# Kernel optimization log

Hardware: AMD Instinct MI355X
Metric: run time of the kernel (lower is better)

## Reference

```python
import jax, jax.numpy as jnp
import numpy as np

N = 1024          # number of rois (single image)
C = 1024          # in_channels
G = 16            # num_groups
PE = 64           # position_embedding_channels
WAVE_LENGTH = 1000.0


def _position_embedding(bboxes, pe_channels, wave_length):
    # bboxes: [N, 4] xyxy. Pairwise geometric features vs all (nongt == all) boxes.
    x1, y1, x2, y2 = jnp.split(bboxes, 4, axis=1)          # each [N,1]
    cx = (x1 + x2) * 0.5
    cy = (y1 + y2) * 0.5
    w = x2 - x1 + 1.0
    h = y2 - y1 + 1.0
    dX = jnp.log(jnp.clip(jnp.abs((cx - cx.T) / w), 1e-3))  # [N,N]
    dY = jnp.log(jnp.clip(jnp.abs((cy - cy.T) / h), 1e-3))
    dW = jnp.log(w / w.T)
    dH = jnp.log(h / h.T)
    pm = jnp.stack([dX, dY, dW, dH], axis=-1)               # [N,N,4]
    feat_range = jnp.arange(pe_channels // 8, dtype=pm.dtype)
    dim_mat = jnp.power(jnp.asarray(wave_length, pm.dtype),
                        (8.0 / pe_channels) * feat_range)    # [pe//8]
    div = (100.0 * pm)[..., None] / dim_mat                  # [N,N,4,pe//8]
    emb = jnp.concatenate([jnp.sin(div), jnp.cos(div)], axis=3)  # [N,N,4,pe//4]
    return emb.reshape(emb.shape[0], emb.shape[1], -1)       # [N,N,pe]


def setup_inputs() -> dict:
    key = jax.random.key(0)
    ks = jax.random.split(key, 10)
    feats = jax.random.normal(ks[0], (N, C), dtype=jnp.float32)
    # realistic boxes: x1,y1 in [0,800), w,h in [1,200)
    x1 = jax.random.uniform(ks[1], (N, 1), minval=0.0, maxval=800.0)
    y1 = jax.random.uniform(ks[2], (N, 1), minval=0.0, maxval=800.0)
    bw = jax.random.uniform(ks[3], (N, 1), minval=1.0, maxval=200.0)
    bh = jax.random.uniform(ks[4], (N, 1), minval=1.0, maxval=200.0)
    rois = jnp.concatenate([jnp.zeros((N, 1)), x1, y1, x1 + bw, y1 + bh], axis=1).astype(jnp.float32)
    Wq = 0.01 * jax.random.normal(ks[5], (C, C), dtype=jnp.float32)
    bq = jnp.zeros((C,), jnp.float32)
    Wk = 0.01 * jax.random.normal(ks[6], (C, C), dtype=jnp.float32)
    bk = jnp.zeros((C,), jnp.float32)
    Wg = 0.01 * jax.random.normal(ks[7], (G, PE), dtype=jnp.float32)   # 1x1 conv PE->G
    bg = jnp.zeros((G,), jnp.float32)
    # grouped 1x1 conv: in=G*C, out=C, groups=G -> weight [C, C]
    limit = np.sqrt(6.0 / (C + C))
    Wv = jax.random.uniform(ks[8], (C, C), minval=-limit, maxval=limit, dtype=jnp.float32)
    bv = jnp.zeros((C,), jnp.float32)
    return {"feats": feats, "rois": rois, "Wq": Wq, "bq": bq, "Wk": Wk, "bk": bk,
            "Wg": Wg, "bg": bg, "Wv": Wv, "bv": bv}


def reference(feats, rois, Wq, bq, Wk, bk, Wg, bg, Wv, bv):
    n, c = feats.shape
    g = Wg.shape[0]
    gc = c // g
    # position embedding computed under no_grad in torch
    emb = jax.lax.stop_gradient(_position_embedding(rois[:, 1:5], Wg.shape[1], WAVE_LENGTH))  # [N,N,PE]
    # 1x1 conv w_g + relu -> geometric attention weight [N, G, M]
    aff_weight = jax.nn.relu(jnp.einsum('nmp,gp->ngm', emb, Wg) + bg[None, :, None])
    q = (feats @ Wq.T + bq).reshape(n, g, gc)   # [N,G,gc]
    k = (feats @ Wk.T + bk).reshape(n, g, gc)   # [M,G,gc] (nongt == all)
    scale = 1.0 / jnp.sqrt(jnp.asarray(gc, jnp.float32))
    aff = jnp.einsum('ngc,mgc->ngm', q, k) * scale            # [N,G,M]
    weighted = jnp.log(jnp.clip(aff_weight, 1e-6)) + aff
    sm = jax.nn.softmax(weighted, axis=2)                      # [N,G,M]
    out = jnp.einsum('ngm,mc->ngc', sm, feats)                 # [N,G,C]
    # grouped 1x1 conv w_v: group g maps its C-dim aggregate to gc channels
    Wv_g = Wv.reshape(g, gc, c)
    rel = jnp.einsum('ngc,gdc->ngd', out, Wv_g).reshape(n, c) + bv
    return rel
```

## Files before the change

### kernel.cpp

```cpp
#include <hip/hip_runtime.h>
#include <math.h>

#define N_ROIS 1024
#define C_DIM  1024

typedef __attribute__((ext_vector_type(8))) short short8;
typedef __attribute__((ext_vector_type(4))) float f32x4;

__device__ __forceinline__ unsigned short f2bf(float x) {
    union { float f; unsigned u; } v; v.f = x;
    unsigned r = v.u + 0x7fffu + ((v.u >> 16) & 1u);
    return (unsigned short)(r >> 16);
}
__device__ __forceinline__ float bf2f(unsigned short u) {
    return __uint_as_float((unsigned)u << 16);
}
__device__ __forceinline__ unsigned cvtpk(float lo, float hi) {
    unsigned r;
    asm("v_cvt_pk_bf16_f32 %0, %1, %2" : "=v"(r) : "v"(lo), "v"(hi));
    return r;
}
__device__ __forceinline__ float sin_rev(float rev) {
    return __builtin_amdgcn_sinf(__builtin_amdgcn_fractf(rev));
}

__global__ __launch_bounds__(256) void cvt_kernel(
    const float* __restrict__ s0, const float* __restrict__ s1,
    const float* __restrict__ s2, const float* __restrict__ s3,
    unsigned short* __restrict__ d0, unsigned short* __restrict__ d1,
    unsigned short* __restrict__ d2, unsigned short* __restrict__ d3)
{
    const float* s; unsigned short* d;
    switch (blockIdx.y) {
        case 0:  s = s0; d = d0; break;
        case 1:  s = s1; d = d1; break;
        case 2:  s = s2; d = d2; break;
        default: s = s3; d = d3; break;
    }
    const int i = (blockIdx.x * 256 + threadIdx.x) * 8;
    float4 a = *(const float4*)&s[i];
    float4 b = *(const float4*)&s[i + 4];
    uint4 o;
    o.x = cvtpk(a.x, a.y); o.y = cvtpk(a.z, a.w);
    o.z = cvtpk(b.x, b.y); o.w = cvtpk(b.z, b.w);
    *(uint4*)&d[i] = o;
}

struct Triples {
    const unsigned short* A[3];
    const unsigned short* B[3];
    unsigned short*       C[3];
    const float*          bias[3];
};

__global__ __launch_bounds__(256) void prep_kernel(
    Triples tr, const float* __restrict__ rois, const float* __restrict__ Wg,
    const float* __restrict__ bg, unsigned short* __restrict__ logw)
{
    __shared__ __align__(16) char smem[24576];
    const int bx = blockIdx.x;
    const int t  = threadIdx.x;
    const int grp = bx / 11, rem = bx % 11;

    if (rem < 3) {
        const int gid = grp * 3 + rem;
        const int z   = gid >> 7;
        const int r3  = gid & 127;
        const int m0 = (r3 >> 3) * 64, n0 = (r3 & 7) * 128;
        const unsigned short* A = tr.A[z];
        const unsigned short* B = tr.B[z];

        const int lane = t & 63, w = t >> 6;
        const int lx = lane & 15, qw = lane >> 4;

#define PGLD(srcp, dstoff) __builtin_amdgcn_global_load_lds( \
        (const __attribute__((address_space(1))) void*)(srcp), \
        (__attribute__((address_space(3))) void*)(smem + (dstoff)), 16, 0, 0)

        const int rsub = lane >> 2;
        const int sg   = ((lane & 3) ^ (rsub & 3)) * 8;
#define STAGE(bb, kk) do { \
        PGLD(A + (size_t)(m0 + w * 16 + rsub) * 1024 + (kk) + sg, \
             (bb) * 4096 + w * 1024 + lane * 16); \
        PGLD(B + (size_t)(n0 + w * 32 + rsub) * 1024 + (kk) + sg, \
             8192 + (bb) * 8192 + (w * 2) * 1024 + lane * 16); \
        PGLD(B + (size_t)(n0 + w * 32 + 16 + rsub) * 1024 + (kk) + sg, \
             8192 + (bb) * 8192 + (w * 2 + 1) * 1024 + lane * 16); \
    } while (0)

        f32x4 acc[2][4];
        const f32x4 z4 = {0.f, 0.f, 0.f, 0.f};
#pragma unroll
        for (int i = 0; i < 2; ++i)
#pragma unroll
            for (int j = 0; j < 4; ++j) acc[i][j] = z4;

        const int wm = (w & 1) * 32, wn = (w >> 1) * 64;
        const int rdsw = (qw ^ (lx & 3)) << 4;

        STAGE(0, 0);
        __syncthreads();

        for (int k0 = 0; k0 < 1024; k0 += 32) {
            const int cur = (k0 >> 5) & 1;
            if (k0 + 32 < 1024) STAGE(cur ^ 1, k0 + 32);
            const char* Ac = smem + cur * 4096;
            const char* Bc = smem + 8192 + cur * 8192;
            short8 af[2], bfr[4];
#pragma unroll
            for (int mi = 0; mi < 2; ++mi)
                af[mi] = *(const short8*)(Ac + (wm + mi * 16 + lx) * 64 + rdsw);
#pragma unroll
            for (int ni = 0; ni < 4; ++ni)
                bfr[ni] = *(const short8*)(Bc + (wn + ni * 16 + lx) * 64 + rdsw);
#pragma unroll
            for (int mi = 0; mi < 2; ++mi)
#pragma unroll
                for (int ni = 0; ni < 4; ++ni)
                    acc[mi][ni] = __builtin_amdgcn_mfma_f32_16x16x32_bf16(
                        af[mi], bfr[ni], acc[mi][ni], 0, 0, 0);
            __syncthreads();
        }
#undef STAGE
#undef PGLD

        const float* bias = tr.bias[z];
        unsigned short* C = tr.C[z];
        const float sc = (z == 0) ? 0.125f : 1.0f;
        const int r0 = qw * 4, cc = lx;
#pragma unroll
        for (int mi = 0; mi < 2; ++mi)
#pragma unroll
            for (int ni = 0; ni < 4; ++ni) {
                const int col = n0 + wn + ni * 16 + cc;
                const float bb = bias ? bias[col] : 0.f;
                const int rowi = m0 + wm + mi * 16 + r0;
                const unsigned p01 = cvtpk((acc[mi][ni][0] + bb) * sc,
                                           (acc[mi][ni][1] + bb) * sc);
                const unsigned p23 = cvtpk((acc[mi][ni][2] + bb) * sc,
                                           (acc[mi][ni][3] + bb) * sc);
                C[(size_t)rowi * 1024 + col]       = (unsigned short)(p01 & 0xffff);
                C[(size_t)(rowi + 1) * 1024 + col] = (unsigned short)(p01 >> 16);
                C[(size_t)(rowi + 2) * 1024 + col] = (unsigned short)(p23 & 0xffff);
                C[(size_t)(rowi + 3) * 1024 + col] = (unsigned short)(p23 >> 16);
            }
    } else {
        unsigned short* wg_s = (unsigned short*)smem;
        float* bg_s = (float*)(smem + 2304);
        float (*mbox)[4] = (float(*)[4])(smem + 2368);
        unsigned short* ptile0 = (unsigned short*)(smem + 6464);
        const int pb = grp * 8 + (rem - 3);
        const int ngrp = pb >> 2;
        const int mc   = (pb & 3) * 256;
        const int lane = t & 63, w = t >> 6;
        const int g = lane & 15, qw = lane >> 4;
        unsigned short* pt = ptile0 + w * 2240;

        if (t < 128) {
            const int gi = t >> 3, c = (t & 7) * 8;
            unsigned short* d = &wg_s[gi * 72 + c];
#pragma unroll
            for (int u2 = 0; u2 < 8; ++u2) d[u2] = f2bf(Wg[gi * 64 + c + u2]);
        }
        if (t < 16) bg_s[t] = bg[t];
        {
            const int m = mc + t;
            const float x1 = rois[m * 5 + 1], y1 = rois[m * 5 + 2];
            const float x2 = rois[m * 5 + 3], y2 = rois[m * 5 + 4];
            mbox[t][0] = (x1 + x2) * 0.5f;
            mbox[t][1] = (y1 + y2) * 0.5f;
            mbox[t][2] = __logf(x2 - x1 + 1.f);
            mbox[t][3] = __logf(y2 - y1 + 1.f);
        }
        const int n = ngrp * 4 + w;
        const float x1 = rois[n * 5 + 1], y1 = rois[n * 5 + 2];
        const float x2 = rois[n * 5 + 3], y2 = rois[n * 5 + 4];
        const float cxn = (x1 + x2) * 0.5f, cyn = (y1 + y2) * 0.5f;
        const float wn = x2 - x1 + 1.f, hn = y2 - y1 + 1.f;
        const float iwn = 1.f / wn, ihn = 1.f / hn;
        const float lwn = __logf(wn), lhn = __logf(hn);
        __syncthreads();

        const float cr = (qw & 1) ? 0.25f : 0.f;
        const int f0 = qw >> 1;
        const short8 bf0 = *(const short8*)&wg_s[g * 72 + qw * 8];
        const short8 bf1 = *(const short8*)&wg_s[g * 72 + qw * 8 + 32];
        const float bgv = bg_s[g];
        const float revd[8] = {15.91549431f, 6.7115081f, 2.8302193f, 1.1934936f,
                               0.5032921f, 0.2122365f, 0.0894993f, 0.0377415f};

        for (int cl = 0; cl < 16; ++cl) {
            float4 mb = *(const float4*)&mbox[cl * 16 + g][0];
            const float p0 = (f0 == 0)
                     ? __logf(fmaxf(fabsf((cxn - mb.x) * iwn), 1e-3f))
                     : __logf(fmaxf(fabsf((cyn - mb.y) * ihn), 1e-3f));
            const float p1 = (f0 == 0) ? (lwn - mb.z) : (lhn - mb.w);
            float s0v[8], s1v[8];
#pragma unroll
            for (int rr = 0; rr < 8; ++rr) {
                const float rv = revd[rr];
                s0v[rr] = sin_rev(fmaf(p0, rv, cr));
                s1v[rr] = sin_rev(fmaf(p1, rv, cr));
            }
            union { uint4 u; short8 s; } a0, a1;
            a0.u.x = cvtpk(s0v[0], s0v[1]); a0.u.y = cvtpk(s0v[2], s0v[3]);
            a0.u.z = cvtpk(s0v[4], s0v[5]); a0.u.w = cvtpk(s0v[6], s0v[7]);
            a1.u.x = cvtpk(s1v[0], s1v[1]); a1.u.y = cvtpk(s1v[2], s1v[3]);
            a1.u.z = cvtpk(s1v[4], s1v[5]); a1.u.w = cvtpk(s1v[6], s1v[7]);
            f32x4 acc = {0.f, 0.f, 0.f, 0.f};
            acc = __builtin_amdgcn_mfma_f32_16x16x32_bf16(a0.s, bf0, acc, 0, 0, 0);
            acc = __builtin_amdgcn_mfma_f32_16x16x32_bf16(a1.s, bf1, acc, 0, 0, 0);
            const float l0 = __logf(fmaxf(acc[0] + bgv, 1e-6f));
            const float l1 = __logf(fmaxf(acc[1] + bgv, 1e-6f));
            const float l2 = __logf(fmaxf(acc[2] + bgv, 1e-6f));
            const float l3 = __logf(fmaxf(acc[3] + bgv, 1e-6f));
            uint2 pk;
            pk.x = cvtpk(l0, l1);
            pk.y = cvtpk(l2, l3);
            *(uint2*)&pt[g * 140 + (cl & 7) * 16 + qw * 4] = pk;

            if ((cl & 7) == 7) {
                const int fl = cl >> 3;
                const int gg = lane >> 2, c4 = lane & 3;
                unsigned short* op = logw + (size_t)n * 16384 + gg * 1024 + mc + fl * 128;
                const unsigned short* rp = &pt[gg * 140];
#pragma unroll
                for (int j = 0; j < 8; ++j) {
                    const int mo = (c4 + j * 4) * 4;
                    *(uint2*)&op[mo] = *(const uint2*)&rp[mo];
                }
            }
        }
    }
}

#define QOFF 0
#define KOFF 8192
#define FOFF 24576
#define LOFF 40960
#define POFF 57344
#define PPAD 72

__global__ __launch_bounds__(256) void attn_kernel(
    const unsigned short* __restrict__ qb, const unsigned short* __restrict__ kb,
    const unsigned short* __restrict__ logw, const unsigned short* __restrict__ FWt,
    const float* __restrict__ bv, float* __restrict__ out)
{
    __shared__ __align__(16) char smem[66560];

    const int t = threadIdx.x;
    const int bid = blockIdx.x;
    const int g  = (bid & 7) * 2 + ((bid >> 3) >> 4);
    const int n0 = ((bid >> 3) & 15) * 64;

    const int lane = t & 63, W = t >> 6;
    const int qw = lane >> 4, lx = lane & 15;
    const int lx7 = lx & 7;
    const int r8 = lane >> 3, u = lane & 7;

#define GLD(srcp, ldsoff) __builtin_amdgcn_global_load_lds( \
        (const __attribute__((address_space(1))) void*)(srcp), \
        (__attribute__((address_space(3))) void*)(smem + (ldsoff)), 16, 0, 0)

#pragma unroll
    for (int j = 0; j < 2; ++j) {
        const int c = W * 2 + j;
        const int r = c * 8 + r8;
        GLD(qb + (size_t)(n0 + r) * 1024 + g * 64 + ((u ^ (r & 7)) * 8),
            QOFF + c * 1024);
        GLD(kb + (size_t)r * 1024 + g * 64 + ((u ^ (r & 7)) * 8),
            KOFF + c * 1024);
        GLD(FWt + (size_t)(g * 64 + r) * 1024 + ((u ^ (r & 7)) * 8),
            FOFF + c * 1024);
        GLD(logw + (size_t)(n0 + r) * 16384 + g * 1024 + (((2 * u) ^ (r & 6)) * 4),
            LOFF + c * 1024);
    }
    __syncthreads();

    const unsigned short* qS = (const unsigned short*)(smem + QOFF);
    const int qrow = W * 16 + lx;
    const short8 bq0 = *(const short8*)(qS + qrow * 64 + ((qw ^ lx7) * 8));
    const short8 bq1 = *(const short8*)(qS + qrow * 64 + (((qw + 4) ^ lx7) * 8));
    unsigned short* Pw = (unsigned short*)(smem + POFF) + W * 16 * PPAD;

    f32x4 acc[4];
    const f32x4 z4 = {0.f, 0.f, 0.f, 0.f};
#pragma unroll
    for (int nb = 0; nb < 4; ++nb) acc[nb] = z4;
    float mrow = -1e30f, srow = 0.f;

    for (int i = 0; i < 16; ++i) {
        const int cur = i & 1;
        if (i < 15) {
            const int mc = (i + 1) * 64;
            const int nxt = cur ^ 1;
#pragma unroll
            for (int j = 0; j < 2; ++j) {
                const int c = W * 2 + j;
                const int r = c * 8 + r8;
                GLD(kb + (size_t)(mc + r) * 1024 + g * 64 + ((u ^ (r & 7)) * 8),
                    KOFF + nxt * 8192 + c * 1024);
                GLD(FWt + (size_t)(g * 64 + r) * 1024 + mc + ((u ^ (r & 7)) * 8),
                    FOFF + nxt * 8192 + c * 1024);
                GLD(logw + (size_t)(n0 + r) * 16384 + g * 1024 + mc
                        + (((2 * u) ^ (r & 6)) * 4),
                    LOFF + nxt * 8192 + c * 1024);
            }
        }

        const unsigned short* Kc = (const unsigned short*)(smem + KOFF + cur * 8192);
        const unsigned short* Fc = (const unsigned short*)(smem + FOFF + cur * 8192);
        const unsigned short* Lc = (const unsigned short*)(smem + LOFF + cur * 8192);

        f32x4 s[4];
#pragma unroll
        for (int tt = 0; tt < 4; ++tt) {
            const unsigned short* kr = Kc + (tt * 16 + lx) * 64;
            short8 a0 = *(const short8*)(kr + ((qw ^ lx7) * 8));
            short8 a1 = *(const short8*)(kr + (((qw + 4) ^ lx7) * 8));
            f32x4 z = z4;
            z = __builtin_amdgcn_mfma_f32_16x16x32_bf16(a0, bq0, z, 0, 0, 0);
            s[tt] = __builtin_amdgcn_mfma_f32_16x16x32_bf16(a1, bq1, z, 0, 0, 0);
        }

        const unsigned short* Lr = Lc + (W * 16 + lx) * 64;
        float v[4][4];
        float cmx = -1e30f;
#pragma unroll
        for (int tt = 0; tt < 4; ++tt) {
            const int off = ((tt * 32 + qw * 8) ^ ((lx & 6) << 3)) >> 1;
            const uint2 lw = *(const uint2*)(Lr + off);
            v[tt][0] = s[tt][0] + bf2f((unsigned short)(lw.x & 0xffff));
            v[tt][1] = s[tt][1] + bf2f((unsigned short)(lw.x >> 16));
            v[tt][2] = s[tt][2] + bf2f((unsigned short)(lw.y & 0xffff));
            v[tt][3] = s[tt][3] + bf2f((unsigned short)(lw.y >> 16));
            cmx = fmaxf(cmx, fmaxf(fmaxf(v[tt][0], v[tt][1]), fmaxf(v[tt][2], v[tt][3])));
        }
        cmx = fmaxf(cmx, __shfl_xor(cmx, 16));
        cmx = fmaxf(cmx, __shfl_xor(cmx, 32));

        const float nm = fmaxf(mrow, cmx);
        const float f  = __expf(mrow - nm);
        mrow = nm;
        srow *= f;
#pragma unroll
        for (int nb = 0; nb < 4; ++nb) {
            acc[nb][0] *= f; acc[nb][1] *= f;
            acc[nb][2] *= f; acc[nb][3] *= f;
        }

#pragma unroll
        for (int tt = 0; tt < 4; ++tt) {
            const float p0 = __expf(v[tt][0] - nm);
            const float p1 = __expf(v[tt][1] - nm);
            const float p2 = __expf(v[tt][2] - nm);
            const float p3 = __expf(v[tt][3] - nm);
            srow += (p0 + p1) + (p2 + p3);
            uint2 pk;
            pk.x = cvtpk(p0, p1);
            pk.y = cvtpk(p2, p3);
            *(uint2*)&Pw[lx * PPAD + tt * 16 + qw * 4] = pk;
        }

#pragma unroll
        for (int ks = 0; ks < 2; ++ks) {
            const short8 ap = *(const short8*)&Pw[lx * PPAD + ks * 32 + qw * 8];
#pragma unroll
            for (int nb = 0; nb < 4; ++nb) {
                const unsigned short* fr = Fc + (nb * 16 + lx) * 64;
                short8 fb = *(const short8*)(fr + (((ks * 4 + qw) ^ lx7) * 8));
                acc[nb] = __builtin_amdgcn_mfma_f32_16x16x32_bf16(fb, ap, acc[nb], 0, 0, 0);
            }
        }

        __syncthreads();
    }

    srow += __shfl_xor(srow, 16);
    srow += __shfl_xor(srow, 32);
    const float inv = 1.f / srow;
    float* Ow = (float*)smem + W * 16 * 68;
#pragma unroll
    for (int nb = 0; nb < 4; ++nb)
#pragma unroll
        for (int r = 0; r < 4; ++r)
            Ow[lx * 68 + nb * 16 + qw * 4 + r] = acc[nb][r] * inv;
    {
        const int row = lane >> 2, d0 = (lane & 3) * 16;
        const float* Orow = (float*)smem + W * 16 * 68 + row * 68;
        float* op = out + (size_t)(n0 + W * 16 + row) * 1024 + g * 64 + d0;
#pragma unroll
        for (int j = 0; j < 4; ++j) {
            float4 o = *(const float4*)(Orow + d0 + j * 4);
            const float4 b4 = *(const float4*)&bv[g * 64 + d0 + j * 4];
            o.x += b4.x; o.y += b4.y; o.z += b4.z; o.w += b4.w;
            *(float4*)(op + j * 4) = o;
        }
    }
#undef GLD
}

extern "C" void kernel_launch(void* const* d_in, const int* in_sizes, int n_in,
                              void* d_out, int out_size, void* d_ws, size_t ws_size,
                              hipStream_t stream)
{
    const float* feats = (const float*)d_in[0];
    const float* rois  = (const float*)d_in[1];
    const float* Wq    = (const float*)d_in[2];
    const float* bq    = (const float*)d_in[3];
    const float* Wk    = (const float*)d_in[4];
    const float* bk    = (const float*)d_in[5];
    const float* Wg    = (const float*)d_in[6];
    const float* bg    = (const float*)d_in[7];
    const float* Wv    = (const float*)d_in[8];
    const float* bv    = (const float*)d_in[9];
    float* out = (float*)d_out;

    char* wsb = (char*)d_ws;
    unsigned short* logwb  = (unsigned short*)(wsb + (0ull  << 20));
    unsigned short* featsb = (unsigned short*)(wsb + (64ull << 20));
    unsigned short* qb     = (unsigned short*)(wsb + (66ull << 20));
    unsigned short* kb     = (unsigned short*)(wsb + (68ull << 20));
    unsigned short* FWtb   = (unsigned short*)(wsb + (70ull << 20));
    unsigned short* Wqb    = (unsigned short*)(wsb + (80ull << 20));
    unsigned short* Wkb    = (unsigned short*)(wsb + (82ull << 20));
    unsigned short* Wvb    = (unsigned short*)(wsb + (84ull << 20));

    cvt_kernel<<<dim3(512, 4), 256, 0, stream>>>(feats, Wq, Wk, Wv,
                                                 featsb, Wqb, Wkb, Wvb);

    Triples tr;
    tr.A[0] = featsb; tr.B[0] = Wqb;    tr.C[0] = qb;   tr.bias[0] = bq;
    tr.A[1] = featsb; tr.B[1] = Wkb;    tr.C[1] = kb;   tr.bias[1] = bk;
    tr.A[2] = Wvb;    tr.B[2] = featsb; tr.C[2] = FWtb; tr.bias[2] = nullptr;
    prep_kernel<<<1408, 256, 0, stream>>>(tr, rois, Wg, bg, logwb);

    attn_kernel<<<256, 256, 0, stream>>>(qb, kb, logwb, FWtb, bv, out);
}
```

Before: 60.67 us.

## Split attention blocks to 32 rows with 2 waves, doubling grid size

The attention kernel now processes 32 query rows per block with 128 threads (2 waves) instead of 64 rows with 4 waves, and launches 512 blocks instead of 256. K and FW tiles are now loaded by two waves (4 chunks each), and the logw buffer shrinks to 32 rows, which cuts shared memory use. This targets under-filling of the MI355X's 256 CUs with only 256 blocks. The cost is that K/FW chunks are reloaded by twice as many blocks, doubling that traffic.

```diff
diff --git a/kernel.cpp b/kernel.cpp
--- a/kernel.cpp
+++ b/kernel.cpp
@@ -235,23 +235,23 @@
 }
 
 #define QOFF 0
-#define KOFF 8192
-#define FOFF 24576
-#define LOFF 40960
-#define POFF 57344
+#define KOFF 4096
+#define FOFF 20480
+#define LOFF 36864
+#define POFF 45056
 #define PPAD 72
 
-__global__ __launch_bounds__(256) void attn_kernel(
+__global__ __launch_bounds__(128) void attn_kernel(
     const unsigned short* __restrict__ qb, const unsigned short* __restrict__ kb,
     const unsigned short* __restrict__ logw, const unsigned short* __restrict__ FWt,
     const float* __restrict__ bv, float* __restrict__ out)
 {
-    __shared__ __align__(16) char smem[66560];
+    __shared__ __align__(16) char smem[49664];
 
     const int t = threadIdx.x;
     const int bid = blockIdx.x;
-    const int g  = (bid & 7) * 2 + ((bid >> 3) >> 4);
-    const int n0 = ((bid >> 3) & 15) * 64;
+    const int g  = (bid & 7) * 2 + ((bid >> 3) >> 5);
+    const int n0 = ((bid >> 3) & 31) * 32;
 
     const int lane = t & 63, W = t >> 6;
     const int qw = lane >> 4, lx = lane & 15;
@@ -261,6 +261,25 @@
 #define GLD(srcp, ldsoff) __builtin_amdgcn_global_load_lds( \
         (const __attribute__((address_space(1))) void*)(srcp), \
         (__attribute__((address_space(3))) void*)(smem + (ldsoff)), 16, 0, 0)
+
+#define CHUNK(mc, buf) do { \
+    _Pragma("unroll") \
+    for (int j = 0; j < 4; ++j) { \
+        const int c = W * 4 + j; \
+        const int r = c * 8 + r8; \
+        GLD(kb + (size_t)((mc) + r) * 1024 + g * 64 + ((u ^ (r & 7)) * 8), \
+            KOFF + (buf) * 8192 + c * 1024); \
+        GLD(FWt + (size_t)(g * 64 + r) * 1024 + (mc) + ((u ^ (r & 7)) * 8), \
+            FOFF + (buf) * 8192 + c * 1024); \
+    } \
+    _Pragma("unroll") \
+    for (int j = 0; j < 2; ++j) { \
+        const int c = W * 2 + j; \
+        const int r = c * 8 + r8; \
+        GLD(logw + (size_t)(n0 + r) * 16384 + g * 1024 + (mc) \
+                + (((2 * u) ^ (r & 6)) * 4), \
+            LOFF + (buf) * 4096 + c * 1024); \
+    } } while (0)
 
 #pragma unroll
     for (int j = 0; j < 2; ++j) {
@@ -268,13 +287,8 @@
         const int r = c * 8 + r8;
         GLD(qb + (size_t)(n0 + r) * 1024 + g * 64 + ((u ^ (r & 7)) * 8),
             QOFF + c * 1024);
-        GLD(kb + (size_t)r * 1024 + g * 64 + ((u ^ (r & 7)) * 8),
-            KOFF + c * 1024);
-        GLD(FWt + (size_t)(g * 64 + r) * 1024 + ((u ^ (r & 7)) * 8),
-            FOFF + c * 1024);
-        GLD(logw + (size_t)(n0 + r) * 16384 + g * 1024 + (((2 * u) ^ (r & 6)) * 4),
-            LOFF + c * 1024);
     }
+    CHUNK(0, 0);
     __syncthreads();
 
     const unsigned short* qS = (const unsigned short*)(smem + QOFF);
@@ -293,24 +307,12 @@
         const int cur = i & 1;
         if (i < 15) {
             const int mc = (i + 1) * 64;
-            const int nxt = cur ^ 1;
-#pragma unroll
-            for (int j = 0; j < 2; ++j) {
-                const int c = W * 2 + j;
-                const int r = c * 8 + r8;
-                GLD(kb + (size_t)(mc + r) * 1024 + g * 64 + ((u ^ (r & 7)) * 8),
-                    KOFF + nxt * 8192 + c * 1024);
-                GLD(FWt + (size_t)(g * 64 + r) * 1024 + mc + ((u ^ (r & 7)) * 8),
-                    FOFF + nxt * 8192 + c * 1024);
-                GLD(logw + (size_t)(n0 + r) * 16384 + g * 1024 + mc
-                        + (((2 * u) ^ (r & 6)) * 4),
-                    LOFF + nxt * 8192 + c * 1024);
-            }
+            CHUNK(mc, cur ^ 1);
         }
 
         const unsigned short* Kc = (const unsigned short*)(smem + KOFF + cur * 8192);
         const unsigned short* Fc = (const unsigned short*)(smem + FOFF + cur * 8192);
-        const unsigned short* Lc = (const unsigned short*)(smem + LOFF + cur * 8192);
+        const unsigned short* Lc = (const unsigned short*)(smem + LOFF + cur * 4096);
 
         f32x4 s[4];
 #pragma unroll
@@ -375,6 +377,7 @@
 
         __syncthreads();
     }
+#undef CHUNK
 
     srow += __shfl_xor(srow, 16);
     srow += __shfl_xor(srow, 32);
@@ -435,5 +438,5 @@
     tr.A[2] = Wvb;    tr.B[2] = featsb; tr.C[2] = FWtb; tr.bias[2] = nullptr;
     prep_kernel<<<1408, 256, 0, stream>>>(tr, rois, Wg, bg, logwb);
 
-    attn_kernel<<<256, 256, 0, stream>>>(qb, kb, logwb, FWtb, bv, out);
-}
+    attn_kernel<<<512, 128, 0, stream>>>(qb, kb, logwb, FWtb, bv, out);
+}
```

After: 64.45 us. 1.06x slower.
